# Performance work log

Hardware: AMD Instinct MI355X
Metric: run time of the kernel (lower is better)

The kernel has to match this reference:

```python
import jax, jax.numpy as jnp
import numpy as np

INPUT_DIM, HIDDEN_DIM, OUTPUT_DIM = 64, 256, 32
BATCH, SEQ = 256, 1024
# AutoNCP(256, 32, sparsity_level=0.5): motor=32, command=max(int(0.4*224),1)=89, inter=135
LAYER_HID = [135, 89, 32]
LAYER_IN = [INPUT_DIM, 135, 89]


def setup_inputs() -> dict:
    key = jax.random.key(0)
    ks = iter(jax.random.split(key, 64))
    d = {}
    d["x"] = jax.random.normal(next(ks), (BATCH, SEQ, INPUT_DIM), dtype=jnp.float32)
    for l, (fin, hid) in enumerate(zip(LAYER_IN, LAYER_HID)):
        sp = jax.random.bernoulli(next(ks), 0.5, (hid, fin))
        d[f"mask{l}"] = jnp.concatenate([sp, jnp.ones((hid, hid), dtype=bool)], axis=1)
        scale = 1.0 / np.sqrt(fin + hid)
        for name in ("W1", "W2", "Wa", "Wb"):
            d[f"{name}_{l}"] = jax.random.normal(next(ks), (hid, fin + hid), dtype=jnp.float32) * scale
        for name in ("b1", "b2", "ba", "bb"):
            d[f"{name}_{l}"] = jnp.zeros((hid,), dtype=jnp.float32)
    d["fc_W"] = jax.random.normal(next(ks), (HIDDEN_DIM, HIDDEN_DIM), dtype=jnp.float32) * (1.0 / np.sqrt(HIDDEN_DIM))
    d["fc_b"] = jnp.zeros((HIDDEN_DIM,), dtype=jnp.float32)
    return d


def _cfc_cell(inp, h, mask, W1, b1, W2, b2, Wa, ba, Wb, bb):
    # ncps CfCCell, mode='default', no backbone, ts = 1.0
    x = jnp.concatenate([inp, h], axis=1)
    m = mask.astype(W1.dtype)
    ff1 = jnp.tanh(x @ (W1 * m).T + b1)
    ff2 = jnp.tanh(x @ (W2 * m).T + b2)
    t = jax.nn.sigmoid(x @ Wa.T + ba + x @ Wb.T + bb)  # sigmoid(t_a*ts + t_b), ts=1
    return ff1 * (1.0 - t) + t * ff2


def _forward(x, masks, layer_params, fc_W, fc_b):
    B = x.shape[0]
    init = tuple(jnp.zeros((B, h), dtype=x.dtype) for h in LAYER_HID)

    def step(carry, xt):
        hs = list(carry)
        inp = xt
        for l in range(3):  # inter -> command -> motor (WiredCfCCell)
            hs[l] = _cfc_cell(inp, hs[l], masks[l], *layer_params[l])
            inp = hs[l]
        return tuple(hs), None

    carry, _ = jax.lax.scan(step, init, jnp.swapaxes(x, 0, 1))  # scan over time [T,B,D]
    hn = jnp.concatenate(carry, axis=1)  # [B, HIDDEN_DIM] full state
    return hn @ fc_W.T + fc_b


def reference(x, mask0, mask1, mask2,
              W1_0, b1_0, W2_0, b2_0, Wa_0, ba_0, Wb_0, bb_0,
              W1_1, b1_1, W2_1, b2_1, Wa_1, ba_1, Wb_1, bb_1,
              W1_2, b1_2, W2_2, b2_2, Wa_2, ba_2, Wb_2, bb_2,
              fc_W, fc_b):
    masks = (mask0, mask1, mask2)
    lp = ((W1_0, b1_0, W2_0, b2_0, Wa_0, ba_0, Wb_0, bb_0),
          (W1_1, b1_1, W2_1, b2_1, Wa_1, ba_1, Wb_1, bb_1),
          (W1_2, b1_2, W2_2, b2_2, Wa_2, ba_2, Wb_2, bb_2))
    return _forward(x, masks, lp, fc_W, fc_b)
```

## Files before the change

kernel.cpp:

```cpp
#include <hip/hip_runtime.h>


typedef _Float16 half2v __attribute__((ext_vector_type(2)));
typedef _Float16 half8v __attribute__((ext_vector_type(8)));

#define NBLK   256
#define NTHR   512
#define TSTEPS 1024
#define KPAD   224
#define WIN    64

struct Ptrs {
    const float* x;
    const unsigned int* msk[3];
    const float* W1[3];
    const float* W2[3];
    const float* Wa[3];
    const float* Wb[3];
    const float* b1[3];
    const float* b2[3];
    const float* ba[3];
    const float* bb[3];
    const float* fcW;
    const float* fcb;
};

__device__ __forceinline__ float fexp2(float x) {
#if __has_builtin(__builtin_amdgcn_exp2f)
    return __builtin_amdgcn_exp2f(x);
#else
    return exp2f(x);
#endif
}
__device__ __forceinline__ float frcp(float x) {
#if __has_builtin(__builtin_amdgcn_rcpf)
    return __builtin_amdgcn_rcpf(x);
#else
    return 1.0f / x;
#endif
}
__device__ __forceinline__ float fsig(float x) {
    return frcp(1.0f + fexp2(-1.442695041f * x));
}
__device__ __forceinline__ float ftanh(float x) {
    return 2.0f * frcp(1.0f + fexp2(-2.885390082f * x)) - 1.0f;
}

#if __has_builtin(__builtin_amdgcn_fdot2)
#define FD(a, b, c) __builtin_amdgcn_fdot2((a), (b), (c), false)
#else
__device__ __forceinline__ float fd_fallback(half2v a, half2v b, float c) {
    return c + (float)a[0] * (float)b[0] + (float)a[1] * (float)b[1];
}
#define FD(a, b, c) fd_fallback((a), (b), (c))
#endif

__device__ __forceinline__ half2v h2(_Float16 a, _Float16 b) { return half2v{a, b}; }

__device__ __forceinline__ float psum(float x) { return x + __shfl_xor(x, 1, 64); }

#define DOJOB(jj_) { \
    const int jm = (jj_) >> 7, jn = (jj_) & 127; \
    const float* Wp = (jm == 0) ? P.W1[0] : (jm == 1) ? P.W2[0] : P.Wa[0]; \
    const float* Wq = P.Wb[0]; \
    const unsigned int* mk0 = P.msk[0]; \
    const int base = jn * 199; \
    half2v wrow[32]; \
    _Pragma("unroll") \
    for (int i2 = 0; i2 < 32; ++i2) { \
        const int k = 2 * i2; \
        float v0 = Wp[base + k], v1 = Wp[base + k + 1]; \
        if (jm == 2) { v0 += Wq[base + k]; v1 += Wq[base + k + 1]; } \
        else { \
            v0 = (mk0[base + k] != 0u) ? v0 : 0.0f; \
            v1 = (mk0[base + k + 1] != 0u) ? v1 : 0.0f; \
        } \
        wrow[i2] = h2((_Float16)v0, (_Float16)v1); \
    } \
    for (int ti = 0; ti < WIN; ++ti) { \
        float acc = 0.0f; \
        _Pragma("unroll") \
        for (int q = 0; q < 8; ++q) { \
            const half8v xq = *(const half8v*)&xwin[ti][8 * q]; \
            acc = FD(h2(xq[0], xq[1]), wrow[4 * q + 0], acc); \
            acc = FD(h2(xq[2], xq[3]), wrow[4 * q + 1], acc); \
            acc = FD(h2(xq[4], xq[5]), wrow[4 * q + 2], acc); \
            acc = FD(h2(xq[6], xq[7]), wrow[4 * q + 3], acc); \
        } \
        U[jm][ti][jn] = (_Float16)acc; \
    } \
}

#define WINDOW_BLOCK(STAGE_, JOBS_) \
    if ((tick & (WIN - 1)) == 0 && tick < TSTEPS) { \
        __syncthreads(); \
        STAGE_ \
        __syncthreads(); \
        JOBS_ \
        __syncthreads(); \
    }

__global__ __launch_bounds__(NTHR)
void cfc_kernel(Ptrs P, float* __restrict__ out) {
    __shared__ __align__(16) _Float16 xc[2][3][KPAD];
    __shared__ __align__(16) float    hn[256];
    __shared__ __align__(16) _Float16 U[3][WIN][128];
    __shared__ __align__(16) _Float16 wa0[128][152];
    __shared__ __align__(16) _Float16 wa1[128][232];
    __shared__ __align__(16) _Float16 xwin[WIN][64];

    const int tid  = threadIdx.x;
    const int b    = blockIdx.x;
    const int unit = tid >> 1;
    const int half = tid & 1;

    {
        int* z = (int*)&xc[0][0][0];
        for (int i = tid; i < 2 * 3 * KPAD / 2; i += NTHR) z[i] = 0;
    }
    __syncthreads();

    const size_t rb = (size_t)b * TSTEPS;

    if (tid < 256) {
        const int n = unit;
        const float* W1p = P.W1[0];
        const float* W2p = P.W2[0];
        const float* Wap = P.Wa[0];
        const float* Wbp = P.Wb[0];
        const int nK = n * 199;

        half2v w1h[36], w2h[36];
#pragma unroll
        for (int i = 0; i < 36; ++i) {
            const int c = 64 + 72 * half + 2 * i;
            float u0 = (c < 199)     ? W1p[nK + c]     : 0.0f;
            float u1 = (c + 1 < 199) ? W1p[nK + c + 1] : 0.0f;
            float v0 = (c < 199)     ? W2p[nK + c]     : 0.0f;
            float v1 = (c + 1 < 199) ? W2p[nK + c + 1] : 0.0f;
            w1h[i] = h2((_Float16)u0, (_Float16)u1);
            w2h[i] = h2((_Float16)v0, (_Float16)v1);
            float a0 = (c < 199)     ? Wap[nK + c] + Wbp[nK + c]         : 0.0f;
            float a1 = (c + 1 < 199) ? Wap[nK + c + 1] + Wbp[nK + c + 1] : 0.0f;
            *(half2v*)&wa0[n][72 * half + 2 * i] = h2((_Float16)a0, (_Float16)a1);
        }
        const float bv1 = P.b1[0][n];
        const float bv2 = P.b2[0][n];
        const float bva = P.ba[0][n] + P.bb[0][n];
        __syncthreads();

        for (int tick = 0; tick < TSTEPS + 2; ++tick) {
            WINDOW_BLOCK(
                if (tid < 64) {
                    for (int ti = 0; ti < WIN; ++ti)
                        xwin[ti][tid] = (_Float16)P.x[(rb + tick + ti) * 64 + tid];
                },
                { DOJOB(tid); if (tid < 64) { DOJOB(320 + tid); } }
            )
            const int s = tick;
            if (s < TSTEPS) {
                const _Float16* srcp = &xc[s & 1][0][64 + 72 * half];
                const _Float16* wvp  = &wa0[n][72 * half];
                float a0 = 0.f, a1 = 0.f, b0 = 0.f, b1 = 0.f, c0 = 0.f, c1 = 0.f;
#pragma unroll
                for (int kb = 0; kb < 9; ++kb) {
                    const half8v xv = *(const half8v*)(srcp + kb * 8);
                    const half8v wv = *(const half8v*)(wvp + kb * 8);
                    const half2v x0 = h2(xv[0], xv[1]), x1 = h2(xv[2], xv[3]);
                    const half2v x2 = h2(xv[4], xv[5]), x3 = h2(xv[6], xv[7]);
                    a0 = FD(x0, w1h[kb * 4 + 0], a0); b0 = FD(x0, w2h[kb * 4 + 0], b0);
                    c0 = FD(x0, h2(wv[0], wv[1]), c0);
                    a1 = FD(x1, w1h[kb * 4 + 1], a1); b1 = FD(x1, w2h[kb * 4 + 1], b1);
                    c1 = FD(x1, h2(wv[2], wv[3]), c1);
                    a0 = FD(x2, w1h[kb * 4 + 2], a0); b0 = FD(x2, w2h[kb * 4 + 2], b0);
                    c0 = FD(x2, h2(wv[4], wv[5]), c0);
                    a1 = FD(x3, w1h[kb * 4 + 3], a1); b1 = FD(x3, w2h[kb * 4 + 3], b1);
                    c1 = FD(x3, h2(wv[6], wv[7]), c1);
                }
                const int tw = s & (WIN - 1);
                const float u1 = (float)U[0][tw][n];
                const float u2 = (float)U[1][tw][n];
                const float ua = (float)U[2][tw][n];
                const float s1 = psum(a0 + a1) + u1 + bv1;
                const float s2 = psum(b0 + b1) + u2 + bv2;
                const float sa = psum(c0 + c1) + ua + bva;
                const float f1 = ftanh(s1);
                const float f2 = ftanh(s2);
                const float tg = fsig(sa);
                const float h  = f1 + tg * (f2 - f1);
                const _Float16 hv = (_Float16)h;
                const int pA = s & 1, pB = (s + 1) & 1;
                if (half == 0) {
                    xc[pA][1][n] = hv;
                    if (s == TSTEPS - 1) hn[n] = h;
                } else {
                    xc[pB][0][64 + n] = hv;
                }
            }
            __syncthreads();
        }
    } else if (tid < 448) {
        int L, n;
        if (unit < 135) { L = 0; n = unit; } else { L = 1; n = unit - 135; }
        const int K    = (L == 0) ? 199 : 224;
        const int HOFF = (L == 0) ? 0 : 135;
        const float* W1p = P.W1[L];
        const float* W2p = P.W2[L];
        const float* Wap = P.Wa[L];
        const float* Wbp = P.Wb[L];
        const unsigned int* mkp = P.msk[L];
        const int nK   = n * K;
        const int koff = 112 * half;
        const int u128 = unit - 128;

        half2v wr1[56], wr2[56];
#pragma unroll
        for (int i = 0; i < 56; ++i) {
            const int k0 = koff + 2 * i, k1 = k0 + 1;
            float u0 = 0.f, u1 = 0.f, v0 = 0.f, v1 = 0.f, a0 = 0.f, a1 = 0.f;
            if (k0 < K) {
                const int idx = nK + k0;
                const float mm = (mkp[idx] != 0u) ? 1.0f : 0.0f;
                u0 = W1p[idx] * mm; v0 = W2p[idx] * mm;
                a0 = Wap[idx] + Wbp[idx];
            }
            if (k1 < K) {
                const int idx = nK + k1;
                const float mm = (mkp[idx] != 0u) ? 1.0f : 0.0f;
                u1 = W1p[idx] * mm; v1 = W2p[idx] * mm;
                a1 = Wap[idx] + Wbp[idx];
            }
            wr1[i] = h2((_Float16)u0, (_Float16)u1);
            wr2[i] = h2((_Float16)v0, (_Float16)v1);
            *(half2v*)&wa1[u128][k0] = h2((_Float16)a0, (_Float16)a1);
        }
        const float bv1 = P.b1[L][n];
        const float bv2 = P.b2[L][n];
        const float bva = P.ba[L][n] + P.bb[L][n];
        __syncthreads();

        for (int tick = 0; tick < TSTEPS + 2; ++tick) {
            WINDOW_BLOCK(;, ;)
            const int s = tick - L;
            if (s >= 0 && s < TSTEPS) {
                const _Float16* srcp = &xc[s & 1][L][koff];
                const _Float16* wvp  = &wa1[u128][koff];
                float a0 = 0.f, a1 = 0.f, b0 = 0.f, b1 = 0.f, c0 = 0.f, c1 = 0.f;
#pragma unroll
                for (int kb = 0; kb < 14; ++kb) {
                    const half8v xv = *(const half8v*)(srcp + kb * 8);
                    const half8v wv = *(const half8v*)(wvp + kb * 8);
                    const half2v x0 = h2(xv[0], xv[1]), x1 = h2(xv[2], xv[3]);
                    const half2v x2 = h2(xv[4], xv[5]), x3 = h2(xv[6], xv[7]);
                    a0 = FD(x0, wr1[kb * 4 + 0], a0); b0 = FD(x0, wr2[kb * 4 + 0], b0);
                    c0 = FD(x0, h2(wv[0], wv[1]), c0);
                    a1 = FD(x1, wr1[kb * 4 + 1], a1); b1 = FD(x1, wr2[kb * 4 + 1], b1);
                    c1 = FD(x1, h2(wv[2], wv[3]), c1);
                    a0 = FD(x2, wr1[kb * 4 + 2], a0); b0 = FD(x2, wr2[kb * 4 + 2], b0);
                    c0 = FD(x2, h2(wv[4], wv[5]), c0);
                    a1 = FD(x3, wr1[kb * 4 + 3], a1); b1 = FD(x3, wr2[kb * 4 + 3], b1);
                    c1 = FD(x3, h2(wv[6], wv[7]), c1);
                }
                const float s1 = psum(a0 + a1) + bv1;
                const float s2 = psum(b0 + b1) + bv2;
                const float sa = psum(c0 + c1) + bva;
                const float f1 = ftanh(s1);
                const float f2 = ftanh(s2);
                const float tg = fsig(sa);
                const float h  = f1 + tg * (f2 - f1);
                const _Float16 hv = (_Float16)h;
                const int pA = s & 1, pB = (s + 1) & 1;
                if (half == 0) {
                    if (L == 0) xc[pA][1][n] = hv; else xc[pA][2][n] = hv;
                    if (s == TSTEPS - 1) hn[HOFF + n] = h;
                } else {
                    if (L == 0) xc[pB][0][64 + n] = hv; else xc[pB][1][135 + n] = hv;
                }
            }
            __syncthreads();
        }
    } else {
        const int n = unit - 224;
        const float* W1p = P.W1[2];
        const float* W2p = P.W2[2];
        const float* Wap = P.Wa[2];
        const float* Wbp = P.Wb[2];
        const unsigned int* mkp = P.msk[2];
        const int nK   = n * 121;
        const int koff = 64 * half;
        const int u128 = unit - 128;

        half2v w1q[32], w2q[32];
#pragma unroll
        for (int i = 0; i < 32; ++i) {
            const int k0 = koff + 2 * i, k1 = k0 + 1;
            float u0 = 0.f, u1 = 0.f, v0 = 0.f, v1 = 0.f, a0 = 0.f, a1 = 0.f;
            if (k0 < 121) {
                const int idx = nK + k0;
                const float mm = (mkp[idx] != 0u) ? 1.0f : 0.0f;
                u0 = W1p[idx] * mm; v0 = W2p[idx] * mm;
                a0 = Wap[idx] + Wbp[idx];
            }
            if (k1 < 121) {
                const int idx = nK + k1;
                const float mm = (mkp[idx] != 0u) ? 1.0f : 0.0f;
                u1 = W1p[idx] * mm; v1 = W2p[idx] * mm;
                a1 = Wap[idx] + Wbp[idx];
            }
            w1q[i] = h2((_Float16)u0, (_Float16)u1);
            w2q[i] = h2((_Float16)v0, (_Float16)v1);
            *(half2v*)&wa1[u128][k0] = h2((_Float16)a0, (_Float16)a1);
        }
        const float bv1 = P.b1[2][n];
        const float bv2 = P.b2[2][n];
        const float bva = P.ba[2][n] + P.bb[2][n];

        const int xlane = tid - 448;
        float xpend = 0.0f;
        xc[0][0][xlane] = (_Float16)P.x[(rb + 0) * 64 + xlane];
        xpend           = P.x[(rb + 1) * 64 + xlane];
        __syncthreads();

        for (int tick = 0; tick < TSTEPS + 2; ++tick) {
            WINDOW_BLOCK(;, DOJOB(tid - 192);)
            if (tick + 1 < TSTEPS)
                xc[(tick + 1) & 1][0][xlane] = (_Float16)xpend;
            if (tick + 2 < TSTEPS)
                xpend = P.x[(rb + (tick + 2)) * 64 + xlane];

            const int s = tick - 2;
            if (s >= 0 && s < TSTEPS) {
                const _Float16* srcp = &xc[s & 1][2][koff];
                const _Float16* wvp  = &wa1[u128][koff];
                float a0 = 0.f, a1 = 0.f, b0 = 0.f, b1 = 0.f, c0 = 0.f, c1 = 0.f;
#pragma unroll
                for (int kb = 0; kb < 8; ++kb) {
                    const half8v xv = *(const half8v*)(srcp + kb * 8);
                    const half8v wv = *(const half8v*)(wvp + kb * 8);
                    const half2v x0 = h2(xv[0], xv[1]), x1 = h2(xv[2], xv[3]);
                    const half2v x2 = h2(xv[4], xv[5]), x3 = h2(xv[6], xv[7]);
                    a0 = FD(x0, w1q[kb * 4 + 0], a0); b0 = FD(x0, w2q[kb * 4 + 0], b0);
                    c0 = FD(x0, h2(wv[0], wv[1]), c0);
                    a1 = FD(x1, w1q[kb * 4 + 1], a1); b1 = FD(x1, w2q[kb * 4 + 1], b1);
                    c1 = FD(x1, h2(wv[2], wv[3]), c1);
                    a0 = FD(x2, w1q[kb * 4 + 2], a0); b0 = FD(x2, w2q[kb * 4 + 2], b0);
                    c0 = FD(x2, h2(wv[4], wv[5]), c0);
                    a1 = FD(x3, w1q[kb * 4 + 3], a1); b1 = FD(x3, w2q[kb * 4 + 3], b1);
                    c1 = FD(x3, h2(wv[6], wv[7]), c1);
                }
                const float s1 = psum(a0 + a1) + bv1;
                const float s2 = psum(b0 + b1) + bv2;
                const float sa = psum(c0 + c1) + bva;
                const float f1 = ftanh(s1);
                const float f2 = ftanh(s2);
                const float tg = fsig(sa);
                const float h  = f1 + tg * (f2 - f1);
                const _Float16 hv = (_Float16)h;
                const int pB = (s + 1) & 1;
                if (half == 0) {
                    if (s == TSTEPS - 1) hn[224 + n] = h;
                } else {
                    xc[pB][2][89 + n] = hv;
                }
            }
            __syncthreads();
        }
    }

    {
        const int o = unit;
        const float4* wr = (const float4*)(P.fcW + (size_t)o * 256 + half * 128);
        const float4* hr = (const float4*)(hn + half * 128);
        float acc = half ? 0.0f : P.fcb[o];
#pragma unroll 8
        for (int d = 0; d < 32; ++d) {
            const float4 a = hr[d];
            const float4 w = wr[d];
            acc += a.x * w.x + a.y * w.y + a.z * w.z + a.w * w.w;
        }
        acc = psum(acc);
        if (half == 0) out[(size_t)b * 256 + o] = acc;
    }
}

extern "C" void kernel_launch(void* const* d_in, const int* in_sizes, int n_in,
                              void* d_out, int out_size, void* d_ws, size_t ws_size,
                              hipStream_t stream) {
    (void)in_sizes; (void)n_in; (void)out_size; (void)d_ws; (void)ws_size;
    Ptrs P;
    P.x = (const float*)d_in[0];
    for (int l = 0; l < 3; ++l) {
        const int base = 1 + l * 9;
        P.msk[l] = (const unsigned int*)d_in[base + 0];
        P.W1[l]  = (const float*)d_in[base + 1];
        P.W2[l]  = (const float*)d_in[base + 2];
        P.Wa[l]  = (const float*)d_in[base + 3];
        P.Wb[l]  = (const float*)d_in[base + 4];
        P.b1[l]  = (const float*)d_in[base + 5];
        P.b2[l]  = (const float*)d_in[base + 6];
        P.ba[l]  = (const float*)d_in[base + 7];
        P.bb[l]  = (const float*)d_in[base + 8];
    }
    P.fcW = (const float*)d_in[28];
    P.fcb = (const float*)d_in[29];

    hipLaunchKernelGGL(cfc_kernel, dim3(NBLK), dim3(NTHR), 0, stream,
                       P, (float*)d_out);
}
```

Baseline: 1.636 ms.

## Halve LDS reads in recurrent dots by sharing x chunks via DPP swaps

Each thread pair now loads alternating 8-element chunks of the state vector from shared memory and swaps them with a DPP row permute, so each lane reads only half of the x data from LDS. Gate weights for layer 0 and layer 2 move from LDS into registers, the U buffer is interleaved so one 4-half load fetches all three precomputed terms, and the shuffle-based pair sum becomes a DPP quad permute. This cuts LDS traffic and latency on the serial per-timestep path, at the cost of more register pressure and a special non-DPP path for one wave whose lanes cross a row boundary.

After: 1.651 ms. Within noise of the previous version (+0.9%).

```diff
diff --git a/kernel.cpp b/kernel.cpp
--- a/kernel.cpp
+++ b/kernel.cpp
@@ -2,7 +2,9 @@
 
 
 typedef _Float16 half2v __attribute__((ext_vector_type(2)));
+typedef _Float16 half4v __attribute__((ext_vector_type(4)));
 typedef _Float16 half8v __attribute__((ext_vector_type(8)));
+typedef int      int4v  __attribute__((ext_vector_type(4)));
 
 #define NBLK   256
 #define NTHR   512
@@ -57,7 +59,55 @@
 
 __device__ __forceinline__ half2v h2(_Float16 a, _Float16 b) { return half2v{a, b}; }
 
-__device__ __forceinline__ float psum(float x) { return x + __shfl_xor(x, 1, 64); }
+__device__ __forceinline__ half8v dpp_xor2(half8v v) {
+    int4v a = __builtin_bit_cast(int4v, v);
+    int4v r;
+    r[0] = __builtin_amdgcn_update_dpp(0, a[0], 0x4E, 0xF, 0xF, true);
+    r[1] = __builtin_amdgcn_update_dpp(0, a[1], 0x4E, 0xF, 0xF, true);
+    r[2] = __builtin_amdgcn_update_dpp(0, a[2], 0x4E, 0xF, 0xF, true);
+    r[3] = __builtin_amdgcn_update_dpp(0, a[3], 0x4E, 0xF, 0xF, true);
+    return __builtin_bit_cast(half8v, r);
+}
+__device__ __forceinline__ float pair_sum(float x) {
+    const int v = __builtin_amdgcn_update_dpp(
+        0, __builtin_bit_cast(int, x), 0xB1, 0xF, 0xF, true);
+    return x + __builtin_bit_cast(float, v);
+}
+
+__device__ __forceinline__ half2v fold2(const float* Wp, const unsigned int* mkp,
+                                        int nK, int K, int k0) {
+    float u0 = 0.f, u1 = 0.f;
+    if (k0 < K)     { u0 = Wp[nK + k0]     * ((mkp[nK + k0]     != 0u) ? 1.0f : 0.0f); }
+    if (k0 + 1 < K) { u1 = Wp[nK + k0 + 1] * ((mkp[nK + k0 + 1] != 0u) ? 1.0f : 0.0f); }
+    return h2((_Float16)u0, (_Float16)u1);
+}
+__device__ __forceinline__ half2v nm2(const float* Wp, int nK, int K, int k0) {
+    float u0 = (k0 < K)     ? Wp[nK + k0]     : 0.0f;
+    float u1 = (k0 + 1 < K) ? Wp[nK + k0 + 1] : 0.0f;
+    return h2((_Float16)u0, (_Float16)u1);
+}
+__device__ __forceinline__ half2v na2(const float* Wa, const float* Wb,
+                                      int nK, int K, int k0) {
+    float u0 = (k0 < K)     ? Wa[nK + k0]     + Wb[nK + k0]     : 0.0f;
+    float u1 = (k0 + 1 < K) ? Wa[nK + k0 + 1] + Wb[nK + k0 + 1] : 0.0f;
+    return h2((_Float16)u0, (_Float16)u1);
+}
+
+#define DOT12R(xv, w1a, w2a, waa, A, B, C) { \
+    const half2v X0 = h2(xv[0], xv[1]), X1 = h2(xv[2], xv[3]); \
+    const half2v X2 = h2(xv[4], xv[5]), X3 = h2(xv[6], xv[7]); \
+    A = FD(X0, (w1a)[0], A); B = FD(X0, (w2a)[0], B); C = FD(X0, (waa)[0], C); \
+    A = FD(X1, (w1a)[1], A); B = FD(X1, (w2a)[1], B); C = FD(X1, (waa)[1], C); \
+    A = FD(X2, (w1a)[2], A); B = FD(X2, (w2a)[2], B); C = FD(X2, (waa)[2], C); \
+    A = FD(X3, (w1a)[3], A); B = FD(X3, (w2a)[3], B); C = FD(X3, (waa)[3], C); }
+
+#define DOT12L(xv, w1a, w2a, wav, A, B, C) { \
+    const half2v X0 = h2(xv[0], xv[1]), X1 = h2(xv[2], xv[3]); \
+    const half2v X2 = h2(xv[4], xv[5]), X3 = h2(xv[6], xv[7]); \
+    A = FD(X0, (w1a)[0], A); B = FD(X0, (w2a)[0], B); C = FD(X0, h2((wav)[0], (wav)[1]), C); \
+    A = FD(X1, (w1a)[1], A); B = FD(X1, (w2a)[1], B); C = FD(X1, h2((wav)[2], (wav)[3]), C); \
+    A = FD(X2, (w1a)[2], A); B = FD(X2, (w2a)[2], B); C = FD(X2, h2((wav)[4], (wav)[5]), C); \
+    A = FD(X3, (w1a)[3], A); B = FD(X3, (w2a)[3], B); C = FD(X3, h2((wav)[6], (wav)[7]), C); }
 
 #define DOJOB(jj_) { \
     const int jm = (jj_) >> 7, jn = (jj_) & 127; \
@@ -87,7 +137,7 @@
             acc = FD(h2(xq[4], xq[5]), wrow[4 * q + 2], acc); \
             acc = FD(h2(xq[6], xq[7]), wrow[4 * q + 3], acc); \
         } \
-        U[jm][ti][jn] = (_Float16)acc; \
+        U[ti][jn][jm] = (_Float16)acc; \
     } \
 }
 
@@ -104,15 +154,15 @@
 void cfc_kernel(Ptrs P, float* __restrict__ out) {
     __shared__ __align__(16) _Float16 xc[2][3][KPAD];
     __shared__ __align__(16) float    hn[256];
-    __shared__ __align__(16) _Float16 U[3][WIN][128];
-    __shared__ __align__(16) _Float16 wa0[128][152];
-    __shared__ __align__(16) _Float16 wa1[128][232];
+    __shared__ __align__(16) _Float16 U[WIN][128][4];
+    __shared__ __align__(16) _Float16 wa1[96][232];
     __shared__ __align__(16) _Float16 xwin[WIN][64];
 
     const int tid  = threadIdx.x;
     const int b    = blockIdx.x;
     const int unit = tid >> 1;
     const int half = tid & 1;
+    const int up   = unit & 1;
 
     {
         int* z = (int*)&xc[0][0][0];
@@ -129,20 +179,31 @@
         const float* Wap = P.Wa[0];
         const float* Wbp = P.Wb[0];
         const int nK = n * 199;
-
-        half2v w1h[36], w2h[36];
-#pragma unroll
-        for (int i = 0; i < 36; ++i) {
-            const int c = 64 + 72 * half + 2 * i;
-            float u0 = (c < 199)     ? W1p[nK + c]     : 0.0f;
-            float u1 = (c + 1 < 199) ? W1p[nK + c + 1] : 0.0f;
-            float v0 = (c < 199)     ? W2p[nK + c]     : 0.0f;
-            float v1 = (c + 1 < 199) ? W2p[nK + c + 1] : 0.0f;
-            w1h[i] = h2((_Float16)u0, (_Float16)u1);
-            w2h[i] = h2((_Float16)v0, (_Float16)v1);
-            float a0 = (c < 199)     ? Wap[nK + c] + Wbp[nK + c]         : 0.0f;
-            float a1 = (c + 1 < 199) ? Wap[nK + c + 1] + Wbp[nK + c + 1] : 0.0f;
-            *(half2v*)&wa0[n][72 * half + 2 * i] = h2((_Float16)a0, (_Float16)a1);
+        const int cb = 64 + 72 * half;
+
+        half2v w1o_[16], w1t_[16], w1l_[4];
+        half2v w2o_[16], w2t_[16], w2l_[4];
+        half2v wao_[16], wat_[16], wal_[4];
+#pragma unroll
+        for (int j = 0; j < 4; ++j) {
+#pragma unroll
+            for (int e = 0; e < 4; ++e) {
+                const int co = cb + (2 * j + up) * 8 + 2 * e;
+                const int ct = cb + (2 * j + 1 - up) * 8 + 2 * e;
+                w1o_[j * 4 + e] = nm2(W1p, nK, 199, co);
+                w1t_[j * 4 + e] = nm2(W1p, nK, 199, ct);
+                w2o_[j * 4 + e] = nm2(W2p, nK, 199, co);
+                w2t_[j * 4 + e] = nm2(W2p, nK, 199, ct);
+                wao_[j * 4 + e] = na2(Wap, Wbp, nK, 199, co);
+                wat_[j * 4 + e] = na2(Wap, Wbp, nK, 199, ct);
+            }
+        }
+#pragma unroll
+        for (int e = 0; e < 4; ++e) {
+            const int cl = cb + 64 + 2 * e;
+            w1l_[e] = nm2(W1p, nK, 199, cl);
+            w2l_[e] = nm2(W2p, nK, 199, cl);
+            wal_[e] = na2(Wap, Wbp, nK, 199, cl);
         }
         const float bv1 = P.b1[0][n];
         const float bv2 = P.b2[0][n];
@@ -159,31 +220,23 @@
             )
             const int s = tick;
             if (s < TSTEPS) {
-                const _Float16* srcp = &xc[s & 1][0][64 + 72 * half];
-                const _Float16* wvp  = &wa0[n][72 * half];
+                const _Float16* srcp = &xc[s & 1][0][cb];
                 float a0 = 0.f, a1 = 0.f, b0 = 0.f, b1 = 0.f, c0 = 0.f, c1 = 0.f;
 #pragma unroll
-                for (int kb = 0; kb < 9; ++kb) {
-                    const half8v xv = *(const half8v*)(srcp + kb * 8);
-                    const half8v wv = *(const half8v*)(wvp + kb * 8);
-                    const half2v x0 = h2(xv[0], xv[1]), x1 = h2(xv[2], xv[3]);
-                    const half2v x2 = h2(xv[4], xv[5]), x3 = h2(xv[6], xv[7]);
-                    a0 = FD(x0, w1h[kb * 4 + 0], a0); b0 = FD(x0, w2h[kb * 4 + 0], b0);
-                    c0 = FD(x0, h2(wv[0], wv[1]), c0);
-                    a1 = FD(x1, w1h[kb * 4 + 1], a1); b1 = FD(x1, w2h[kb * 4 + 1], b1);
-                    c1 = FD(x1, h2(wv[2], wv[3]), c1);
-                    a0 = FD(x2, w1h[kb * 4 + 2], a0); b0 = FD(x2, w2h[kb * 4 + 2], b0);
-                    c0 = FD(x2, h2(wv[4], wv[5]), c0);
-                    a1 = FD(x3, w1h[kb * 4 + 3], a1); b1 = FD(x3, w2h[kb * 4 + 3], b1);
-                    c1 = FD(x3, h2(wv[6], wv[7]), c1);
-                }
-                const int tw = s & (WIN - 1);
-                const float u1 = (float)U[0][tw][n];
-                const float u2 = (float)U[1][tw][n];
-                const float ua = (float)U[2][tw][n];
-                const float s1 = psum(a0 + a1) + u1 + bv1;
-                const float s2 = psum(b0 + b1) + u2 + bv2;
-                const float sa = psum(c0 + c1) + ua + bva;
+                for (int j = 0; j < 4; ++j) {
+                    const half8v xo = *(const half8v*)(srcp + (2 * j + up) * 8);
+                    const half8v xt = dpp_xor2(xo);
+                    DOT12R(xo, &w1o_[4 * j], &w2o_[4 * j], &wao_[4 * j], a0, b0, c0);
+                    DOT12R(xt, &w1t_[4 * j], &w2t_[4 * j], &wat_[4 * j], a1, b1, c1);
+                }
+                {
+                    const half8v xl = *(const half8v*)(srcp + 64);
+                    DOT12R(xl, w1l_, w2l_, wal_, a0, b0, c0);
+                }
+                const half4v uv = *(const half4v*)&U[s & (WIN - 1)][n][0];
+                const float s1 = pair_sum(a0 + a1) + (float)uv[0] + bv1;
+                const float s2 = pair_sum(b0 + b1) + (float)uv[1] + bv2;
+                const float sa = pair_sum(c0 + c1) + (float)uv[2] + bva;
                 const float f1 = ftanh(s1);
                 const float f2 = ftanh(s2);
                 const float tg = fsig(sa);
@@ -212,27 +265,22 @@
         const int nK   = n * K;
         const int koff = 112 * half;
         const int u128 = unit - 128;
-
-        half2v wr1[56], wr2[56];
-#pragma unroll
-        for (int i = 0; i < 56; ++i) {
-            const int k0 = koff + 2 * i, k1 = k0 + 1;
-            float u0 = 0.f, u1 = 0.f, v0 = 0.f, v1 = 0.f, a0 = 0.f, a1 = 0.f;
-            if (k0 < K) {
-                const int idx = nK + k0;
-                const float mm = (mkp[idx] != 0u) ? 1.0f : 0.0f;
-                u0 = W1p[idx] * mm; v0 = W2p[idx] * mm;
-                a0 = Wap[idx] + Wbp[idx];
-            }
-            if (k1 < K) {
-                const int idx = nK + k1;
-                const float mm = (mkp[idx] != 0u) ? 1.0f : 0.0f;
-                u1 = W1p[idx] * mm; v1 = W2p[idx] * mm;
-                a1 = Wap[idx] + Wbp[idx];
-            }
-            wr1[i] = h2((_Float16)u0, (_Float16)u1);
-            wr2[i] = h2((_Float16)v0, (_Float16)v1);
-            *(half2v*)&wa1[u128][k0] = h2((_Float16)a0, (_Float16)a1);
+        const bool direct = ((tid >> 6) == 4);
+
+        half2v w1o[28], w1t[28], w2o[28], w2t[28];
+#pragma unroll
+        for (int j = 0; j < 7; ++j) {
+#pragma unroll
+            for (int e = 0; e < 4; ++e) {
+                const int co = koff + (2 * j + up) * 8 + 2 * e;
+                const int ct = koff + (2 * j + 1 - up) * 8 + 2 * e;
+                w1o[j * 4 + e] = fold2(W1p, mkp, nK, K, co);
+                w1t[j * 4 + e] = fold2(W1p, mkp, nK, K, ct);
+                w2o[j * 4 + e] = fold2(W2p, mkp, nK, K, co);
+                w2t[j * 4 + e] = fold2(W2p, mkp, nK, K, ct);
+                *(half2v*)&wa1[u128][co] = na2(Wap, Wbp, nK, K, co);
+                *(half2v*)&wa1[u128][ct] = na2(Wap, Wbp, nK, K, ct);
+            }
         }
         const float bv1 = P.b1[L][n];
         const float bv2 = P.b2[L][n];
@@ -244,26 +292,32 @@
             const int s = tick - L;
             if (s >= 0 && s < TSTEPS) {
                 const _Float16* srcp = &xc[s & 1][L][koff];
-                const _Float16* wvp  = &wa1[u128][koff];
+                const _Float16* wap  = &wa1[u128][koff];
                 float a0 = 0.f, a1 = 0.f, b0 = 0.f, b1 = 0.f, c0 = 0.f, c1 = 0.f;
-#pragma unroll
-                for (int kb = 0; kb < 14; ++kb) {
-                    const half8v xv = *(const half8v*)(srcp + kb * 8);
-                    const half8v wv = *(const half8v*)(wvp + kb * 8);
-                    const half2v x0 = h2(xv[0], xv[1]), x1 = h2(xv[2], xv[3]);
-                    const half2v x2 = h2(xv[4], xv[5]), x3 = h2(xv[6], xv[7]);
-                    a0 = FD(x0, wr1[kb * 4 + 0], a0); b0 = FD(x0, wr2[kb * 4 + 0], b0);
-                    c0 = FD(x0, h2(wv[0], wv[1]), c0);
-                    a1 = FD(x1, wr1[kb * 4 + 1], a1); b1 = FD(x1, wr2[kb * 4 + 1], b1);
-                    c1 = FD(x1, h2(wv[2], wv[3]), c1);
-                    a0 = FD(x2, wr1[kb * 4 + 2], a0); b0 = FD(x2, wr2[kb * 4 + 2], b0);
-                    c0 = FD(x2, h2(wv[4], wv[5]), c0);
-                    a1 = FD(x3, wr1[kb * 4 + 3], a1); b1 = FD(x3, wr2[kb * 4 + 3], b1);
-                    c1 = FD(x3, h2(wv[6], wv[7]), c1);
-                }
-                const float s1 = psum(a0 + a1) + bv1;
-                const float s2 = psum(b0 + b1) + bv2;
-                const float sa = psum(c0 + c1) + bva;
+                if (!direct) {
+#pragma unroll
+                    for (int j = 0; j < 7; ++j) {
+                        const half8v xo = *(const half8v*)(srcp + (2 * j + up) * 8);
+                        const half8v xt = dpp_xor2(xo);
+                        const half8v wo = *(const half8v*)(wap + (2 * j + up) * 8);
+                        const half8v wt = *(const half8v*)(wap + (2 * j + 1 - up) * 8);
+                        DOT12L(xo, &w1o[4 * j], &w2o[4 * j], wo, a0, b0, c0);
+                        DOT12L(xt, &w1t[4 * j], &w2t[4 * j], wt, a1, b1, c1);
+                    }
+                } else {
+#pragma unroll
+                    for (int j = 0; j < 7; ++j) {
+                        const half8v xo = *(const half8v*)(srcp + (2 * j + up) * 8);
+                        const half8v xt = *(const half8v*)(srcp + (2 * j + 1 - up) * 8);
+                        const half8v wo = *(const half8v*)(wap + (2 * j + up) * 8);
+                        const half8v wt = *(const half8v*)(wap + (2 * j + 1 - up) * 8);
+                        DOT12L(xo, &w1o[4 * j], &w2o[4 * j], wo, a0, b0, c0);
+                        DOT12L(xt, &w1t[4 * j], &w2t[4 * j], wt, a1, b1, c1);
+                    }
+                }
+                const float s1 = pair_sum(a0 + a1) + bv1;
+                const float s2 = pair_sum(b0 + b1) + bv2;
+                const float sa = pair_sum(c0 + c1) + bva;
                 const float f1 = ftanh(s1);
                 const float f2 = ftanh(s2);
                 const float tg = fsig(sa);
@@ -288,28 +342,21 @@
         const unsigned int* mkp = P.msk[2];
         const int nK   = n * 121;
         const int koff = 64 * half;
-        const int u128 = unit - 128;
-
-        half2v w1q[32], w2q[32];
-#pragma unroll
-        for (int i = 0; i < 32; ++i) {
-            const int k0 = koff + 2 * i, k1 = k0 + 1;
-            float u0 = 0.f, u1 = 0.f, v0 = 0.f, v1 = 0.f, a0 = 0.f, a1 = 0.f;
-            if (k0 < 121) {
-                const int idx = nK + k0;
-                const float mm = (mkp[idx] != 0u) ? 1.0f : 0.0f;
-                u0 = W1p[idx] * mm; v0 = W2p[idx] * mm;
-                a0 = Wap[idx] + Wbp[idx];
-            }
-            if (k1 < 121) {
-                const int idx = nK + k1;
-                const float mm = (mkp[idx] != 0u) ? 1.0f : 0.0f;
-                u1 = W1p[idx] * mm; v1 = W2p[idx] * mm;
-                a1 = Wap[idx] + Wbp[idx];
-            }
-            w1q[i] = h2((_Float16)u0, (_Float16)u1);
-            w2q[i] = h2((_Float16)v0, (_Float16)v1);
-            *(half2v*)&wa1[u128][k0] = h2((_Float16)a0, (_Float16)a1);
+
+        half2v w1o_[16], w1t_[16], w2o_[16], w2t_[16], wao_[16], wat_[16];
+#pragma unroll
+        for (int j = 0; j < 4; ++j) {
+#pragma unroll
+            for (int e = 0; e < 4; ++e) {
+                const int co = koff + (2 * j + up) * 8 + 2 * e;
+                const int ct = koff + (2 * j + 1 - up) * 8 + 2 * e;
+                w1o_[j * 4 + e] = fold2(W1p, mkp, nK, 121, co);
+                w1t_[j * 4 + e] = fold2(W1p, mkp, nK, 121, ct);
+                w2o_[j * 4 + e] = fold2(W2p, mkp, nK, 121, co);
+                w2t_[j * 4 + e] = fold2(W2p, mkp, nK, 121, ct);
+                wao_[j * 4 + e] = na2(Wap, Wbp, nK, 121, co);
+                wat_[j * 4 + e] = na2(Wap, Wbp, nK, 121, ct);
+            }
         }
         const float bv1 = P.b1[2][n];
         const float bv2 = P.b2[2][n];
@@ -331,26 +378,17 @@
             const int s = tick - 2;
             if (s >= 0 && s < TSTEPS) {
                 const _Float16* srcp = &xc[s & 1][2][koff];
-                const _Float16* wvp  = &wa1[u128][koff];
                 float a0 = 0.f, a1 = 0.f, b0 = 0.f, b1 = 0.f, c0 = 0.f, c1 = 0.f;
 #pragma unroll
-                for (int kb = 0; kb < 8; ++kb) {
-                    const half8v xv = *(const half8v*)(srcp + kb * 8);
-                    const half8v wv = *(const half8v*)(wvp + kb * 8);
-                    const half2v x0 = h2(xv[0], xv[1]), x1 = h2(xv[2], xv[3]);
-                    const half2v x2 = h2(xv[4], xv[5]), x3 = h2(xv[6], xv[7]);
-                    a0 = FD(x0, w1q[kb * 4 + 0], a0); b0 = FD(x0, w2q[kb * 4 + 0], b0);
-                    c0 = FD(x0, h2(wv[0], wv[1]), c0);
-                    a1 = FD(x1, w1q[kb * 4 + 1], a1); b1 = FD(x1, w2q[kb * 4 + 1], b1);
-                    c1 = FD(x1, h2(wv[2], wv[3]), c1);
-                    a0 = FD(x2, w1q[kb * 4 + 2], a0); b0 = FD(x2, w2q[kb * 4 + 2], b0);
-                    c0 = FD(x2, h2(wv[4], wv[5]), c0);
-                    a1 = FD(x3, w1q[kb * 4 + 3], a1); b1 = FD(x3, w2q[kb * 4 + 3], b1);
-                    c1 = FD(x3, h2(wv[6], wv[7]), c1);
-                }
-                const float s1 = psum(a0 + a1) + bv1;
-                const float s2 = psum(b0 + b1) + bv2;
-                const float sa = psum(c0 + c1) + bva;
+                for (int j = 0; j < 4; ++j) {
+                    const half8v xo = *(const half8v*)(srcp + (2 * j + up) * 8);
+                    const half8v xt = dpp_xor2(xo);
+                    DOT12R(xo, &w1o_[4 * j], &w2o_[4 * j], &wao_[4 * j], a0, b0, c0);
+                    DOT12R(xt, &w1t_[4 * j], &w2t_[4 * j], &wat_[4 * j], a1, b1, c1);
+                }
+                const float s1 = pair_sum(a0 + a1) + bv1;
+                const float s2 = pair_sum(b0 + b1) + bv2;
+                const float sa = pair_sum(c0 + c1) + bva;
                 const float f1 = ftanh(s1);
                 const float f2 = ftanh(s2);
                 const float tg = fsig(sa);
@@ -378,7 +416,7 @@
             const float4 w = wr[d];
             acc += a.x * w.x + a.y * w.y + a.z * w.z + a.w * w.w;
         }
-        acc = psum(acc);
+        acc = pair_sum(acc);
         if (half == 0) out[(size_t)b * 256 + o] = acc;
     }
 }
```
